# Kernel optimization log

Hardware: AMD Instinct MI355X
Metric: run time of the kernel (lower is better)

Reference implementation:

```python
import jax, jax.numpy as jnp
import numpy as np

H = 16      # num_heads
D = 64      # internal_emb_dim (head dim)
E = 1024    # q/kv input embedding dim
NEG_INF = float('-inf')


def setup_inputs() -> dict:
    key = jax.random.key(0)
    ks = jax.random.split(key, 10)
    B, S = 2, 2048
    sc_in = 1.0 / np.sqrt(E)            # kaiming-uniform-ish scale
    sc_h = 1.0 / np.sqrt(H * D)
    return {
        'x':    jax.random.normal(ks[0], (B, S, E), jnp.float32),
        'ln_g': jnp.ones((E,), jnp.float32),
        'ln_b': jnp.zeros((E,), jnp.float32),
        # weights stored [in, out] (transpose of torch layout), biases zero-init per module
        'wq': jax.random.uniform(ks[1], (E, H * D), jnp.float32, -sc_in, sc_in),
        'bq': jnp.zeros((H * D,), jnp.float32),
        'wk': jax.random.uniform(ks[2], (E, H * D), jnp.float32, -sc_in, sc_in),
        'bk': jnp.zeros((H * D,), jnp.float32),
        'wv': jax.random.uniform(ks[3], (E, H * D), jnp.float32, -sc_in, sc_in),
        'bv': jnp.zeros((H * D,), jnp.float32),
        'w0': jax.random.uniform(ks[4], (H * D, E), jnp.float32, -sc_h, sc_h),
        'b0': jnp.zeros((E,), jnp.float32),
    }


def _layer_norm(x, g, b, eps=1e-5):
    mu = jnp.mean(x, axis=-1, keepdims=True)
    var = jnp.mean(jnp.square(x - mu), axis=-1, keepdims=True)
    return (x - mu) * jax.lax.rsqrt(var + eps) * g + b


def reference(x, ln_g, ln_b, wq, bq, wk, bk, wv, bv, w0, b0):
    B, S, _ = x.shape
    residual = x
    xn = _layer_norm(x, ln_g, ln_b)
    # projections -> [B, H, S, D]
    q = (xn @ wq + bq).reshape(B, S, H, D).transpose(0, 2, 1, 3)
    k = (xn @ wk + bk).reshape(B, S, H, D).transpose(0, 2, 1, 3)
    v = (xn @ wv + bv).reshape(B, S, H, D).transpose(0, 2, 1, 3)
    scores = jnp.einsum('bhqd,bhkd->bhqk', q, k) / jnp.sqrt(jnp.float32(D))
    # custom mask: strictly lower triangle (j < i) filled with -inf
    mask = jnp.tril(jnp.ones((S, S), bool), k=-1)
    scores = jnp.where(mask, NEG_INF, scores)
    a = jax.nn.softmax(scores, axis=-1)
    h = jnp.einsum('bhqk,bhkd->bhqd', a, v)
    h = h.transpose(0, 2, 1, 3).reshape(B, S, H * D)
    return h @ w0 + b0 + residual
```

## Files before the change

kernel.cpp:

```cpp
#include <hip/hip_runtime.h>
#include <hip/hip_bf16.h>
#include <stdint.h>

#define S_LEN 2048
#define E_DIM 1024
#define NHEAD 16
#define DHEAD 64
#define NB 2
#define NROWS (NB * S_LEN)

typedef __attribute__((ext_vector_type(8))) short bf16x8;
typedef __attribute__((ext_vector_type(4))) float f32x4;

__device__ __forceinline__ unsigned short f2b(float f) {
    union { __hip_bfloat16 h; unsigned short u; } cv;
    cv.h = __float2bfloat16(f);
    return cv.u;
}

__device__ __forceinline__ void gload_lds16(const void* g, void* l) {
    __builtin_amdgcn_global_load_lds(
        (const __attribute__((address_space(1))) unsigned int*)g,
        (__attribute__((address_space(3))) unsigned int*)l, 16, 0, 0);
}

__global__ __launch_bounds__(256) void wtrans_kernel(
    const float* __restrict__ wq, const float* __restrict__ wk,
    const float* __restrict__ wv, const float* __restrict__ w0,
    unsigned short* __restrict__ wqT, unsigned short* __restrict__ wkT,
    unsigned short* __restrict__ wvT, unsigned short* __restrict__ w0T) {
    const int z = blockIdx.z;
    const float* W = (z == 0) ? wq : (z == 1) ? wk : (z == 2) ? wv : w0;
    unsigned short* WT = (z == 0) ? wqT : (z == 1) ? wkT : (z == 2) ? wvT : w0T;
    const int k0 = blockIdx.x * 64;
    const int n0 = blockIdx.y * 64;
    __shared__ float tile[64][69];
    const int t = threadIdx.x;
    const int rowq = t >> 4;
    const int cc4 = (t & 15) * 4;
    #pragma unroll
    for (int rr = 0; rr < 4; ++rr) {
        const int r = rr * 16 + rowq;
        const float4 v = *reinterpret_cast<const float4*>(W + (size_t)(k0 + r) * E_DIM + n0 + cc4);
        tile[r][cc4 + 0] = v.x; tile[r][cc4 + 1] = v.y;
        tile[r][cc4 + 2] = v.z; tile[r][cc4 + 3] = v.w;
    }
    __syncthreads();
    #pragma unroll
    for (int rr = 0; rr < 4; ++rr) {
        const int n = rr * 16 + rowq;
        ushort4 o;
        o.x = f2b(tile[cc4 + 0][n]);
        o.y = f2b(tile[cc4 + 1][n]);
        o.z = f2b(tile[cc4 + 2][n]);
        o.w = f2b(tile[cc4 + 3][n]);
        *reinterpret_cast<ushort4*>(WT + (size_t)(n0 + n) * E_DIM + k0 + cc4) = o;
    }
}

__global__ __launch_bounds__(256) void ln_kernel(const float* __restrict__ x,
    const float* __restrict__ g, const float* __restrict__ bt,
    unsigned short* __restrict__ xn) {
    const int row = blockIdx.x;
    const int t = threadIdx.x;
    const float4 v = reinterpret_cast<const float4*>(x + (size_t)row * E_DIM)[t];
    float s  = v.x + v.y + v.z + v.w;
    float ss = v.x * v.x + v.y * v.y + v.z * v.z + v.w * v.w;
    #pragma unroll
    for (int off = 32; off > 0; off >>= 1) {
        s  += __shfl_down(s, off);
        ss += __shfl_down(ss, off);
    }
    __shared__ float red[8];
    if ((t & 63) == 0) { red[t >> 6] = s; red[(t >> 6) + 4] = ss; }
    __syncthreads();
    s  = red[0] + red[1] + red[2] + red[3];
    ss = red[4] + red[5] + red[6] + red[7];
    const float mu  = s * (1.0f / E_DIM);
    const float var = ss * (1.0f / E_DIM) - mu * mu;
    const float rs  = rsqrtf(var + 1e-5f);
    const float4 gv = reinterpret_cast<const float4*>(g)[t];
    const float4 bv = reinterpret_cast<const float4*>(bt)[t];
    ushort4 o;
    o.x = f2b((v.x - mu) * rs * gv.x + bv.x);
    o.y = f2b((v.y - mu) * rs * gv.y + bv.y);
    o.z = f2b((v.z - mu) * rs * gv.z + bv.z);
    o.w = f2b((v.w - mu) * rs * gv.w + bv.w);
    reinterpret_cast<ushort4*>(xn + (size_t)row * E_DIM)[t] = o;
}

__device__ __forceinline__ void gemm128_mainloop(
    const unsigned short* __restrict__ A, const unsigned short* __restrict__ BT,
    int m0, int n0, unsigned short* As, unsigned short* Bs, f32x4 acc[4][4]) {
    const int t = threadIdx.x;
    const int l = t & 63;
    const int w = t >> 6;
    const int wr = w >> 1, wc = w & 1;
    const int lr = l >> 3;
    const int gs = (l & 7) ^ lr;
    const int il = l & 15;
    const int kq = l >> 4;

    for (int kt = 0; kt < E_DIM; kt += 64) {
        __syncthreads();
        #pragma unroll
        for (int c = 0; c < 4; ++c) {
            const int cc = w * 4 + c;
            gload_lds16(A + (size_t)(m0 + cc * 8 + lr) * E_DIM + kt + gs * 8, As + cc * 512);
        }
        #pragma unroll
        for (int c = 0; c < 4; ++c) {
            const int cc = w * 4 + c;
            gload_lds16(BT + (size_t)(n0 + cc * 8 + lr) * E_DIM + kt + gs * 8, Bs + cc * 512);
        }
        __syncthreads();
        #pragma unroll
        for (int ks = 0; ks < 2; ++ks) {
            bf16x8 af[4], bfr[4];
            #pragma unroll
            for (int mi = 0; mi < 4; ++mi) {
                const int r = wr * 64 + mi * 16 + il;
                af[mi] = *reinterpret_cast<const bf16x8*>(As + r * 64 + ((ks * 4 + kq) ^ (r & 7)) * 8);
            }
            #pragma unroll
            for (int ni = 0; ni < 4; ++ni) {
                const int r = wc * 64 + ni * 16 + il;
                bfr[ni] = *reinterpret_cast<const bf16x8*>(Bs + r * 64 + ((ks * 4 + kq) ^ (r & 7)) * 8);
            }
            #pragma unroll
            for (int mi = 0; mi < 4; ++mi)
                #pragma unroll
                for (int ni = 0; ni < 4; ++ni)
                    acc[mi][ni] = __builtin_amdgcn_mfma_f32_16x16x32_bf16(af[mi], bfr[ni], acc[mi][ni], 0, 0, 0);
        }
    }
}

__global__ __launch_bounds__(256) void qkv_kernel(
    const unsigned short* __restrict__ xn,
    const unsigned short* __restrict__ wqT, const float* __restrict__ bq,
    const unsigned short* __restrict__ wkT, const float* __restrict__ bk,
    const unsigned short* __restrict__ wvT, const float* __restrict__ bv,
    unsigned short* __restrict__ qo, unsigned short* __restrict__ ko,
    unsigned short* __restrict__ vo) {
    __shared__ __align__(16) unsigned short As[8192];
    __shared__ __align__(16) unsigned short Bs[8192];
    const int mat = blockIdx.z;
    const unsigned short* BT = (mat == 0) ? wqT : (mat == 1) ? wkT : wvT;
    const float* bias = (mat == 0) ? bq : (mat == 1) ? bk : bv;
    const int m0 = blockIdx.x * 128, n0 = blockIdx.y * 128;

    const f32x4 ZERO = {0.f, 0.f, 0.f, 0.f};
    f32x4 acc[4][4];
    #pragma unroll
    for (int i = 0; i < 4; ++i)
        #pragma unroll
        for (int j = 0; j < 4; ++j) acc[i][j] = ZERO;

    gemm128_mainloop(xn, BT, m0, n0, As, Bs, acc);

    const int t = threadIdx.x, l = t & 63, w = t >> 6;
    const int wr = w >> 1, wc = w & 1;
    const int il = l & 15, kq = l >> 4;
    const int b = m0 >> 11;
    const float qsc = (mat == 0) ? 0.125f : 1.0f;
    unsigned short* outp = (mat == 0) ? qo : ko;

    #pragma unroll
    for (int ni = 0; ni < 4; ++ni) {
        const int n = n0 + wc * 64 + ni * 16 + il;
        const int h = n >> 6, d = n & 63;
        const float bb = bias[n];
        #pragma unroll
        for (int mi = 0; mi < 4; ++mi) {
            const int mbase = m0 + wr * 64 + mi * 16 + kq * 4;
            const int sbase = mbase & (S_LEN - 1);
            if (mat == 2) {
                ushort4 o;
                o.x = f2b(acc[mi][ni][0] + bb);
                o.y = f2b(acc[mi][ni][1] + bb);
                o.z = f2b(acc[mi][ni][2] + bb);
                o.w = f2b(acc[mi][ni][3] + bb);
                *reinterpret_cast<ushort4*>(vo + ((size_t)(b * NHEAD + h) * DHEAD + d) * S_LEN + sbase) = o;
            } else {
                #pragma unroll
                for (int r = 0; r < 4; ++r)
                    outp[((size_t)(b * NHEAD + h) * S_LEN + sbase + r) * DHEAD + d] =
                        f2b((acc[mi][ni][r] + bb) * qsc);
            }
        }
    }
}

__device__ __forceinline__ void attn_tile128(
    const unsigned short* __restrict__ Kc, const unsigned short* __restrict__ Vc,
    unsigned short* __restrict__ Pw, const bf16x8* qf,
    float& m, float& lsum, f32x4* o,
    int il, int kq, int w, int qi0, int kt0, bool do_mask) {
    const f32x4 ZERO = {0.f, 0.f, 0.f, 0.f};
    f32x4 s[8];
    #pragma unroll
    for (int nf = 0; nf < 8; ++nf) s[nf] = ZERO;
    __builtin_amdgcn_s_setprio(1);
    #pragma unroll
    for (int ks = 0; ks < 2; ++ks)
        #pragma unroll
        for (int nf = 0; nf < 8; ++nf) {
            const int j = nf * 16 + il;
            const bf16x8 kf = *reinterpret_cast<const bf16x8*>(
                Kc + j * 64 + (((ks * 4 + kq) ^ (il & 7)) * 8));
            s[nf] = __builtin_amdgcn_mfma_f32_16x16x32_bf16(kf, qf[ks], s[nf], 0, 0, 0);
        }
    __builtin_amdgcn_s_setprio(0);
    if (do_mask) {
        const int i = qi0 + w * 16 + il;
        #pragma unroll
        for (int nf = 0; nf < 8; ++nf)
            #pragma unroll
            for (int r = 0; r < 4; ++r) {
                const int j = kt0 + nf * 16 + kq * 4 + r;
                if (j < i) s[nf][r] = -INFINITY;
            }
    }
    float tnf[8];
    #pragma unroll
    for (int nf = 0; nf < 8; ++nf)
        tnf[nf] = fmaxf(fmaxf(s[nf][0], s[nf][1]), fmaxf(s[nf][2], s[nf][3]));
    float tm = fmaxf(fmaxf(fmaxf(tnf[0], tnf[1]), fmaxf(tnf[2], tnf[3])),
                     fmaxf(fmaxf(tnf[4], tnf[5]), fmaxf(tnf[6], tnf[7])));
    tm = fmaxf(tm, __shfl_xor(tm, 16));
    tm = fmaxf(tm, __shfl_xor(tm, 32));

    float sc = 1.0f;
    const bool resc = __any(tm > m + 8.0f);
    if (resc) {
        const float nm = fmaxf(m, tm);
        sc = __expf(m - nm);
        m = nm;
    }

    float ps0 = 0.f, ps1 = 0.f;
    #pragma unroll
    for (int nf = 0; nf < 8; ++nf) {
        const float e0 = __expf(s[nf][0] - m);
        const float e1 = __expf(s[nf][1] - m);
        const float e2 = __expf(s[nf][2] - m);
        const float e3 = __expf(s[nf][3] - m);
        ps0 += e0 + e1; ps1 += e2 + e3;
        ushort4 pk;
        pk.x = f2b(e0); pk.y = f2b(e1); pk.z = f2b(e2); pk.w = f2b(e3);
        *reinterpret_cast<ushort4*>(
            Pw + il * 128 + (((2 * nf + (kq >> 1)) ^ il) << 3) + ((kq & 1) << 2)) = pk;
    }
    float ps = ps0 + ps1;
    ps += __shfl_xor(ps, 16);
    ps += __shfl_xor(ps, 32);
    lsum = lsum * sc + ps;

    if (resc) {
        #pragma unroll
        for (int r = 0; r < 4; ++r) {
            const float scq = __shfl(sc, kq * 4 + r);
            #pragma unroll
            for (int nf = 0; nf < 4; ++nf) o[nf][r] *= scq;
        }
    }

    __builtin_amdgcn_s_setprio(1);
    #pragma unroll
    for (int ks = 0; ks < 4; ++ks) {
        const bf16x8 pa = *reinterpret_cast<const bf16x8*>(
            Pw + il * 128 + (((ks * 4 + kq) ^ il) << 3));
        #pragma unroll
        for (int nf = 0; nf < 4; ++nf) {
            const int dl = nf * 16 + il;
            const bf16x8 vf = *reinterpret_cast<const bf16x8*>(
                Vc + dl * 128 + (((ks * 4 + kq) ^ il) << 3));
            o[nf] = __builtin_amdgcn_mfma_f32_16x16x32_bf16(pa, vf, o[nf], 0, 0, 0);
        }
    }
    __builtin_amdgcn_s_setprio(0);
}

__global__ __launch_bounds__(256) void attn_kernel(
    const unsigned short* __restrict__ q,
    const unsigned short* __restrict__ k,
    const unsigned short* __restrict__ vt,
    unsigned short* __restrict__ hb) {
    __shared__ __align__(16) unsigned short Ks[2][8192];
    __shared__ __align__(16) unsigned short Vs[2][8192];
    __shared__ __align__(16) unsigned short Ps[8192];
    const int qtA = blockIdx.x;
    const int bh  = blockIdx.y;
    const int qiA = qtA * 64;
    const int qiB = (31 - qtA) * 64;
    const int startA = qiA & ~127;
    const int startB = qiB & ~127;
    const unsigned short* qp = q + (size_t)bh * S_LEN * DHEAD;
    const unsigned short* kp = k + (size_t)bh * S_LEN * DHEAD;
    const unsigned short* vp = vt + (size_t)bh * DHEAD * S_LEN;
    const int t = threadIdx.x, l = t & 63, w = t >> 6;
    const int il = l & 15, kq = l >> 4;
    const int lr = l >> 3, kls = l & 7;
    const int vr = l >> 4, vs = l & 15;

    auto stage = [&](int buf, int kt) {
        #pragma unroll
        for (int c = 0; c < 4; ++c) {
            const int cc = w * 4 + c;
            const int krow = cc * 8 + lr;
            gload_lds16(kp + (size_t)(kt + krow) * DHEAD + (kls ^ lr) * 8, &Ks[buf][cc * 512]);
            const int vrow = cc * 4 + vr;
            gload_lds16(vp + (size_t)vrow * S_LEN + kt + (vs ^ (vrow & 15)) * 8, &Vs[buf][cc * 512]);
        }
    };

    const f32x4 ZERO = {0.f, 0.f, 0.f, 0.f};
    bf16x8 qfA[2], qfB[2];
    {
        const int rA = qiA + w * 16 + il;
        const int rB = qiB + w * 16 + il;
        qfA[0] = *reinterpret_cast<const bf16x8*>(qp + (size_t)rA * DHEAD + kq * 8);
        qfA[1] = *reinterpret_cast<const bf16x8*>(qp + (size_t)rA * DHEAD + 32 + kq * 8);
        qfB[0] = *reinterpret_cast<const bf16x8*>(qp + (size_t)rB * DHEAD + kq * 8);
        qfB[1] = *reinterpret_cast<const bf16x8*>(qp + (size_t)rB * DHEAD + 32 + kq * 8);
    }

    float mA = -INFINITY, lA = 0.f, mB = -INFINITY, lB = 0.f;
    f32x4 oA[4], oB[4];
    #pragma unroll
    for (int nf = 0; nf < 4; ++nf) { oA[nf] = ZERO; oB[nf] = ZERO; }

    unsigned short* Pw = Ps + w * 2048;

    stage(0, startA);
    __syncthreads();
    int cur = 0;

    for (int kt0 = startA; kt0 < S_LEN; kt0 += 128) {
        if (kt0 + 128 < S_LEN) stage(cur ^ 1, kt0 + 128);
        attn_tile128(Ks[cur], Vs[cur], Pw, qfA, mA, lA, oA, il, kq, w, qiA, kt0, kt0 == startA);
        if (kt0 >= startB)
            attn_tile128(Ks[cur], Vs[cur], Pw, qfB, mB, lB, oB, il, kq, w, qiB, kt0, kt0 == startB);
        __syncthreads();
        cur ^= 1;
    }

    const int b = bh >> 4, hh = bh & 15;
    const float rvA = 1.0f / lA, rvB = 1.0f / lB;
    float rlA[4], rlB[4];
    #pragma unroll
    for (int r = 0; r < 4; ++r) {
        rlA[r] = __shfl(rvA, kq * 4 + r);
        rlB[r] = __shfl(rvB, kq * 4 + r);
    }
    #pragma unroll
    for (int nf = 0; nf < 4; ++nf) {
        const int col = hh * 64 + nf * 16 + il;
        #pragma unroll
        for (int r = 0; r < 4; ++r) {
            const int rowA = qiA + w * 16 + kq * 4 + r;
            const int rowB = qiB + w * 16 + kq * 4 + r;
            hb[(size_t)(b * S_LEN + rowA) * E_DIM + col] = f2b(oA[nf][r] * rlA[r]);
            hb[(size_t)(b * S_LEN + rowB) * E_DIM + col] = f2b(oB[nf][r] * rlB[r]);
        }
    }
}

__global__ __launch_bounds__(256) void oproj_kernel(
    const unsigned short* __restrict__ hbuf, const unsigned short* __restrict__ w0T,
    const float* __restrict__ b0, const float* __restrict__ x,
    float* __restrict__ out) {
    __shared__ __align__(16) unsigned short As[8192];
    __shared__ __align__(16) unsigned short Bs[8192];
    const int m0 = blockIdx.x * 128, n0 = blockIdx.y * 128;

    const f32x4 ZERO = {0.f, 0.f, 0.f, 0.f};
    f32x4 acc[4][4];
    #pragma unroll
    for (int i = 0; i < 4; ++i)
        #pragma unroll
        for (int j = 0; j < 4; ++j) acc[i][j] = ZERO;

    gemm128_mainloop(hbuf, w0T, m0, n0, As, Bs, acc);

    const int t = threadIdx.x, l = t & 63, w = t >> 6;
    const int wr = w >> 1, wc = w & 1;
    const int il = l & 15, kq = l >> 4;
    #pragma unroll
    for (int ni = 0; ni < 4; ++ni) {
        const int n = n0 + wc * 64 + ni * 16 + il;
        const float bb = b0[n];
        #pragma unroll
        for (int mi = 0; mi < 4; ++mi) {
            const int mbase = m0 + wr * 64 + mi * 16 + kq * 4;
            #pragma unroll
            for (int r = 0; r < 4; ++r) {
                const size_t idx = (size_t)(mbase + r) * E_DIM + n;
                out[idx] = acc[mi][ni][r] + bb + x[idx];
            }
        }
    }
}

extern "C" void kernel_launch(void* const* d_in, const int* in_sizes, int n_in,
                              void* d_out, int out_size, void* d_ws, size_t ws_size,
                              hipStream_t stream) {
    (void)in_sizes; (void)n_in; (void)out_size; (void)ws_size;
    const float* x    = (const float*)d_in[0];
    const float* ln_g = (const float*)d_in[1];
    const float* ln_b = (const float*)d_in[2];
    const float* wq   = (const float*)d_in[3];
    const float* bq   = (const float*)d_in[4];
    const float* wk   = (const float*)d_in[5];
    const float* bk   = (const float*)d_in[6];
    const float* wv   = (const float*)d_in[7];
    const float* bv   = (const float*)d_in[8];
    const float* w0   = (const float*)d_in[9];
    const float* b0   = (const float*)d_in[10];

    uint8_t* ws = (uint8_t*)d_ws;
    unsigned short* xnb = (unsigned short*)(ws);
    unsigned short* qb  = (unsigned short*)(ws + (8u  << 20));
    unsigned short* kb  = (unsigned short*)(ws + (16u << 20));
    unsigned short* vtb = (unsigned short*)(ws + (24u << 20));
    unsigned short* wqT = (unsigned short*)(ws + (32u << 20));
    unsigned short* wkT = (unsigned short*)(ws + (34u << 20));
    unsigned short* wvT = (unsigned short*)(ws + (36u << 20));
    unsigned short* w0T = (unsigned short*)(ws + (38u << 20));
    unsigned short* hbf = xnb;

    hipLaunchKernelGGL(wtrans_kernel, dim3(16, 16, 4), dim3(256), 0, stream,
                       wq, wk, wv, w0, wqT, wkT, wvT, w0T);
    hipLaunchKernelGGL(ln_kernel, dim3(NROWS), dim3(256), 0, stream, x, ln_g, ln_b, xnb);
    hipLaunchKernelGGL(qkv_kernel, dim3(32, 8, 3), dim3(256), 0, stream,
                       xnb, wqT, bq, wkT, bk, wvT, bv, qb, kb, vtb);
    hipLaunchKernelGGL(attn_kernel, dim3(16, 32), dim3(256), 0, stream, qb, kb, vtb, hbf);
    hipLaunchKernelGGL(oproj_kernel, dim3(32, 8), dim3(256), 0, stream,
                       hbf, w0T, b0, x, (float*)d_out);
}
```

Before: 214.0 us.

## Swap MFMA operands for Q/K stores, register-stage KV, pad P buffer

For the Q and K projections, the MFMA operands are swapped so each lane holds four consecutive head-dim values, which allows vectorized ushort4 stores and a float4 bias load in place of scalar scattered stores. The attention kernel drops double-buffered direct-to-LDS loads. It now prefetches the next K/V tile into registers and writes them to a single LDS buffer after a barrier, which halves K/V LDS use but adds a second barrier and extra VGPRs. The P scratch buffer changes from an XOR swizzle to a padded row stride, read back as two 8-byte loads, with an explicit lgkmcnt wait before the PV stage.

```diff
diff --git a/kernel.cpp b/kernel.cpp
--- a/kernel.cpp
+++ b/kernel.cpp
@@ -10,6 +10,7 @@
 #define NROWS (NB * S_LEN)
 
 typedef __attribute__((ext_vector_type(8))) short bf16x8;
+typedef __attribute__((ext_vector_type(4))) short bf16x4;
 typedef __attribute__((ext_vector_type(4))) float f32x4;
 
 __device__ __forceinline__ unsigned short f2b(float f) {
@@ -89,6 +90,7 @@
     reinterpret_cast<ushort4*>(xn + (size_t)row * E_DIM)[t] = o;
 }
 
+template<bool SWAP>
 __device__ __forceinline__ void gemm128_mainloop(
     const unsigned short* __restrict__ A, const unsigned short* __restrict__ BT,
     int m0, int n0, unsigned short* As, unsigned short* Bs, f32x4 acc[4][4]) {
@@ -130,8 +132,12 @@
             #pragma unroll
             for (int mi = 0; mi < 4; ++mi)
                 #pragma unroll
-                for (int ni = 0; ni < 4; ++ni)
-                    acc[mi][ni] = __builtin_amdgcn_mfma_f32_16x16x32_bf16(af[mi], bfr[ni], acc[mi][ni], 0, 0, 0);
+                for (int ni = 0; ni < 4; ++ni) {
+                    if constexpr (SWAP)
+                        acc[mi][ni] = __builtin_amdgcn_mfma_f32_16x16x32_bf16(bfr[ni], af[mi], acc[mi][ni], 0, 0, 0);
+                    else
+                        acc[mi][ni] = __builtin_amdgcn_mfma_f32_16x16x32_bf16(af[mi], bfr[ni], acc[mi][ni], 0, 0, 0);
+                }
         }
     }
 }
@@ -157,36 +163,48 @@
         #pragma unroll
         for (int j = 0; j < 4; ++j) acc[i][j] = ZERO;
 
-    gemm128_mainloop(xn, BT, m0, n0, As, Bs, acc);
-
     const int t = threadIdx.x, l = t & 63, w = t >> 6;
     const int wr = w >> 1, wc = w & 1;
     const int il = l & 15, kq = l >> 4;
     const int b = m0 >> 11;
-    const float qsc = (mat == 0) ? 0.125f : 1.0f;
-    unsigned short* outp = (mat == 0) ? qo : ko;
-
-    #pragma unroll
-    for (int ni = 0; ni < 4; ++ni) {
-        const int n = n0 + wc * 64 + ni * 16 + il;
-        const int h = n >> 6, d = n & 63;
-        const float bb = bias[n];
-        #pragma unroll
-        for (int mi = 0; mi < 4; ++mi) {
-            const int mbase = m0 + wr * 64 + mi * 16 + kq * 4;
-            const int sbase = mbase & (S_LEN - 1);
-            if (mat == 2) {
+
+    if (mat == 2) {
+        gemm128_mainloop<false>(xn, BT, m0, n0, As, Bs, acc);
+        #pragma unroll
+        for (int ni = 0; ni < 4; ++ni) {
+            const int n = n0 + wc * 64 + ni * 16 + il;
+            const int h = n >> 6, d = n & 63;
+            const float bb = bias[n];
+            #pragma unroll
+            for (int mi = 0; mi < 4; ++mi) {
+                const int mbase = m0 + wr * 64 + mi * 16 + kq * 4;
+                const int sbase = mbase & (S_LEN - 1);
                 ushort4 o;
                 o.x = f2b(acc[mi][ni][0] + bb);
                 o.y = f2b(acc[mi][ni][1] + bb);
                 o.z = f2b(acc[mi][ni][2] + bb);
                 o.w = f2b(acc[mi][ni][3] + bb);
                 *reinterpret_cast<ushort4*>(vo + ((size_t)(b * NHEAD + h) * DHEAD + d) * S_LEN + sbase) = o;
-            } else {
-                #pragma unroll
-                for (int r = 0; r < 4; ++r)
-                    outp[((size_t)(b * NHEAD + h) * S_LEN + sbase + r) * DHEAD + d] =
-                        f2b((acc[mi][ni][r] + bb) * qsc);
+            }
+        }
+    } else {
+        gemm128_mainloop<true>(xn, BT, m0, n0, As, Bs, acc);
+        const float qsc = (mat == 0) ? 0.125f : 1.0f;
+        unsigned short* outp = (mat == 0) ? qo : ko;
+        #pragma unroll
+        for (int ni = 0; ni < 4; ++ni) {
+            const int nbase = n0 + wc * 64 + ni * 16 + kq * 4;
+            const int h = nbase >> 6, d0 = nbase & 63;
+            const float4 b4 = *reinterpret_cast<const float4*>(bias + nbase);
+            #pragma unroll
+            for (int mi = 0; mi < 4; ++mi) {
+                const int srow = (m0 + wr * 64 + mi * 16 + il) & (S_LEN - 1);
+                ushort4 o;
+                o.x = f2b((acc[mi][ni][0] + b4.x) * qsc);
+                o.y = f2b((acc[mi][ni][1] + b4.y) * qsc);
+                o.z = f2b((acc[mi][ni][2] + b4.z) * qsc);
+                o.w = f2b((acc[mi][ni][3] + b4.w) * qsc);
+                *reinterpret_cast<ushort4*>(outp + ((size_t)(b * NHEAD + h) * S_LEN + srow) * DHEAD + d0) = o;
             }
         }
     }
@@ -249,8 +267,7 @@
         ps0 += e0 + e1; ps1 += e2 + e3;
         ushort4 pk;
         pk.x = f2b(e0); pk.y = f2b(e1); pk.z = f2b(e2); pk.w = f2b(e3);
-        *reinterpret_cast<ushort4*>(
-            Pw + il * 128 + (((2 * nf + (kq >> 1)) ^ il) << 3) + ((kq & 1) << 2)) = pk;
+        *reinterpret_cast<ushort4*>(Pw + il * 132 + nf * 16 + kq * 4) = pk;
     }
     float ps = ps0 + ps1;
     ps += __shfl_xor(ps, 16);
@@ -266,11 +283,13 @@
         }
     }
 
+    asm volatile("s_waitcnt lgkmcnt(0)" ::: "memory");
     __builtin_amdgcn_s_setprio(1);
     #pragma unroll
     for (int ks = 0; ks < 4; ++ks) {
-        const bf16x8 pa = *reinterpret_cast<const bf16x8*>(
-            Pw + il * 128 + (((ks * 4 + kq) ^ il) << 3));
+        const bf16x4 plo = *reinterpret_cast<const bf16x4*>(Pw + il * 132 + (ks * 4 + kq) * 8);
+        const bf16x4 phi = *reinterpret_cast<const bf16x4*>(Pw + il * 132 + (ks * 4 + kq) * 8 + 4);
+        const bf16x8 pa = __builtin_shufflevector(plo, phi, 0, 1, 2, 3, 4, 5, 6, 7);
         #pragma unroll
         for (int nf = 0; nf < 4; ++nf) {
             const int dl = nf * 16 + il;
@@ -287,9 +306,9 @@
     const unsigned short* __restrict__ k,
     const unsigned short* __restrict__ vt,
     unsigned short* __restrict__ hb) {
-    __shared__ __align__(16) unsigned short Ks[2][8192];
-    __shared__ __align__(16) unsigned short Vs[2][8192];
-    __shared__ __align__(16) unsigned short Ps[8192];
+    __shared__ __align__(16) unsigned short Ks[8192];
+    __shared__ __align__(16) unsigned short Vs[8192];
+    __shared__ __align__(16) unsigned short Ps[8448];
     const int qtA = blockIdx.x;
     const int bh  = blockIdx.y;
     const int qiA = qtA * 64;
@@ -304,15 +323,28 @@
     const int lr = l >> 3, kls = l & 7;
     const int vr = l >> 4, vs = l & 15;
 
-    auto stage = [&](int buf, int kt) {
+    uint4 kreg[4], vreg[4];
+    auto loadKV = [&](int kt) {
         #pragma unroll
         for (int c = 0; c < 4; ++c) {
             const int cc = w * 4 + c;
             const int krow = cc * 8 + lr;
-            gload_lds16(kp + (size_t)(kt + krow) * DHEAD + (kls ^ lr) * 8, &Ks[buf][cc * 512]);
+            kreg[c] = *reinterpret_cast<const uint4*>(
+                kp + (size_t)(kt + krow) * DHEAD + (kls ^ lr) * 8);
             const int vrow = cc * 4 + vr;
-            gload_lds16(vp + (size_t)vrow * S_LEN + kt + (vs ^ (vrow & 15)) * 8, &Vs[buf][cc * 512]);
-        }
+            vreg[c] = *reinterpret_cast<const uint4*>(
+                vp + (size_t)vrow * S_LEN + kt + (vs ^ (vrow & 15)) * 8);
+        }
+    };
+    auto writeK = [&]() {
+        #pragma unroll
+        for (int c = 0; c < 4; ++c)
+            *reinterpret_cast<uint4*>(&Ks[(w * 4 + c) * 512 + l * 8]) = kreg[c];
+    };
+    auto writeV = [&]() {
+        #pragma unroll
+        for (int c = 0; c < 4; ++c)
+            *reinterpret_cast<uint4*>(&Vs[(w * 4 + c) * 512 + l * 8]) = vreg[c];
     };
 
     const f32x4 ZERO = {0.f, 0.f, 0.f, 0.f};
@@ -331,19 +363,21 @@
     #pragma unroll
     for (int nf = 0; nf < 4; ++nf) { oA[nf] = ZERO; oB[nf] = ZERO; }
 
-    unsigned short* Pw = Ps + w * 2048;
-
-    stage(0, startA);
+    unsigned short* Pw = Ps + w * 2112;
+
+    loadKV(startA);
+    writeK(); writeV();
     __syncthreads();
-    int cur = 0;
 
     for (int kt0 = startA; kt0 < S_LEN; kt0 += 128) {
-        if (kt0 + 128 < S_LEN) stage(cur ^ 1, kt0 + 128);
-        attn_tile128(Ks[cur], Vs[cur], Pw, qfA, mA, lA, oA, il, kq, w, qiA, kt0, kt0 == startA);
+        const bool more = (kt0 + 128 < S_LEN);
+        if (more) loadKV(kt0 + 128);
+        attn_tile128(Ks, Vs, Pw, qfA, mA, lA, oA, il, kq, w, qiA, kt0, kt0 == startA);
         if (kt0 >= startB)
-            attn_tile128(Ks[cur], Vs[cur], Pw, qfB, mB, lB, oB, il, kq, w, qiB, kt0, kt0 == startB);
+            attn_tile128(Ks, Vs, Pw, qfB, mB, lB, oB, il, kq, w, qiB, kt0, kt0 == startB);
         __syncthreads();
-        cur ^= 1;
+        if (more) { writeK(); writeV(); }
+        __syncthreads();
     }
 
     const int b = bh >> 4, hh = bh & 15;
@@ -382,7 +416,7 @@
         #pragma unroll
         for (int j = 0; j < 4; ++j) acc[i][j] = ZERO;
 
-    gemm128_mainloop(hbuf, w0T, m0, n0, As, Bs, acc);
+    gemm128_mainloop<false>(hbuf, w0T, m0, n0, As, Bs, acc);
 
     const int t = threadIdx.x, l = t & 63, w = t >> 6;
     const int wr = w >> 1, wc = w & 1;
```

After: 259.8 us. 1.21x slower.
